# Performance work log

Hardware: AMD Instinct MI355X
Metric: run time of the kernel (lower is better)

## Reference

```python
import jax, jax.numpy as jnp
import numpy as np


def _gcn_conv(x, edge_index, W, b):
    # PyG GCNConv: linear transform, add self-loops, symmetric deg^{-1/2} norm,
    # scatter-add aggregation from source (row) into target (col), then bias.
    N = x.shape[0]
    h = x @ W  # [N, out]
    loops = jnp.arange(N, dtype=edge_index.dtype)
    row = jnp.concatenate([edge_index[0], loops])  # sources j
    col = jnp.concatenate([edge_index[1], loops])  # targets i
    deg = jax.ops.segment_sum(jnp.ones_like(col, dtype=h.dtype), col, num_segments=N)
    dinv = jnp.where(deg > 0, jax.lax.rsqrt(deg), 0.0)
    norm = dinv[row] * dinv[col]  # [E+N]
    msgs = norm[:, None] * h[row]  # gather + scale
    out = jax.ops.segment_sum(msgs, col, num_segments=N)  # scatter-add
    return out + b


def setup_inputs() -> dict:
    key = jax.random.key(0)
    k1, k2, k3, k4 = jax.random.split(key, 4)
    N, E, F, H = 100000, 3200000, 128, 64
    x = jax.random.normal(k1, (N, F), dtype=jnp.float32)
    edge_index = jax.random.randint(k2, (2, E), 0, N, dtype=jnp.int64)
    W1 = jax.random.normal(k3, (F, H), dtype=jnp.float32) * (1.0 / np.sqrt(F))
    b1 = jnp.zeros((H,), dtype=jnp.float32)
    W2 = jax.random.normal(k4, (H, 1), dtype=jnp.float32) * (1.0 / np.sqrt(H))
    b2 = jnp.zeros((1,), dtype=jnp.float32)
    return {"x": x, "edge_index": edge_index, "W1": W1, "b1": b1, "W2": W2, "b2": b2}


def reference(x, edge_index, W1, b1, W2, b2):
    # eval mode: dropout is identity
    h = _gcn_conv(x, edge_index, W1, b1)
    h = jax.nn.relu(h)
    h = _gcn_conv(h, edge_index, W2, b2)  # [N, 1]
    return jnp.mean(h, axis=0)  # [1]
```

## Files before the change

kernel.cpp:

```cpp
#include <hip/hip_runtime.h>
#include <hip/hip_bf16.h>
#include <stdint.h>


#define F_IN 128
#define H_DIM 64
#define BKT_SH 7
#define BKT_SZ 128
#define MAXBKT 1024
#define PWG 256
#define PTHR 256
#define FINBLK 2048

typedef int   i4 __attribute__((ext_vector_type(4)));
typedef float f4 __attribute__((ext_vector_type(4)));

__device__ __forceinline__ float2 bfp(unsigned int u) {
    return make_float2(__uint_as_float(u << 16), __uint_as_float(u & 0xffff0000u));
}

__global__ __launch_bounds__(PTHR) void k_hist1(const int* __restrict__ col,
                                                int* __restrict__ histG,
                                                int E, int nbkt, int chunk) {
    __shared__ int h[MAXBKT];
    for (int i = threadIdx.x; i < nbkt; i += PTHR) h[i] = 0;
    __syncthreads();
    int s = blockIdx.x * chunk, e = min(E, s + chunk);
    if (s < e) {
        int s4 = s >> 2, e4 = e >> 2;
        const i4* c4 = (const i4*)col;
        int t = s4 + threadIdx.x;
        for (; t + 3 * PTHR < e4; t += 4 * PTHR) {
            i4 a = __builtin_nontemporal_load(c4 + t);
            i4 b = __builtin_nontemporal_load(c4 + t + PTHR);
            i4 c = __builtin_nontemporal_load(c4 + t + 2 * PTHR);
            i4 d = __builtin_nontemporal_load(c4 + t + 3 * PTHR);
            atomicAdd(&h[a.x >> BKT_SH], 1); atomicAdd(&h[a.y >> BKT_SH], 1);
            atomicAdd(&h[a.z >> BKT_SH], 1); atomicAdd(&h[a.w >> BKT_SH], 1);
            atomicAdd(&h[b.x >> BKT_SH], 1); atomicAdd(&h[b.y >> BKT_SH], 1);
            atomicAdd(&h[b.z >> BKT_SH], 1); atomicAdd(&h[b.w >> BKT_SH], 1);
            atomicAdd(&h[c.x >> BKT_SH], 1); atomicAdd(&h[c.y >> BKT_SH], 1);
            atomicAdd(&h[c.z >> BKT_SH], 1); atomicAdd(&h[c.w >> BKT_SH], 1);
            atomicAdd(&h[d.x >> BKT_SH], 1); atomicAdd(&h[d.y >> BKT_SH], 1);
            atomicAdd(&h[d.z >> BKT_SH], 1); atomicAdd(&h[d.w >> BKT_SH], 1);
        }
        for (; t < e4; t += PTHR) {
            i4 a = __builtin_nontemporal_load(c4 + t);
            atomicAdd(&h[a.x >> BKT_SH], 1); atomicAdd(&h[a.y >> BKT_SH], 1);
            atomicAdd(&h[a.z >> BKT_SH], 1); atomicAdd(&h[a.w >> BKT_SH], 1);
        }
        for (int i = (e4 << 2) + threadIdx.x; i < e; i += PTHR)
            atomicAdd(&h[col[i] >> BKT_SH], 1);
    }
    __syncthreads();
    for (int i = threadIdx.x; i < nbkt; i += PTHR)
        histG[(size_t)i * PWG + blockIdx.x] = h[i];
}

__global__ __launch_bounds__(PWG) void k_hscan_a(int* __restrict__ histG,
                                                 int* __restrict__ total, int nbkt) {
    __shared__ int s[PWG];
    int b = blockIdx.x, t = threadIdx.x;
    int v = histG[(size_t)b * PWG + t];
    s[t] = v;
    __syncthreads();
    for (int d = 1; d < PWG; d <<= 1) {
        int a = (t >= d) ? s[t - d] : 0;
        __syncthreads();
        s[t] += a;
        __syncthreads();
    }
    histG[(size_t)b * PWG + t] = s[t] - v;
    if (t == PWG - 1) total[b] = s[t];
}

__global__ __launch_bounds__(1024) void k_hscan_b(const int* __restrict__ total,
                                                  int* __restrict__ bstart, int nbkt) {
    __shared__ int s[1024];
    int t = threadIdx.x;
    int v = (t < nbkt) ? total[t] : 0;
    s[t] = v;
    __syncthreads();
    for (int d = 1; d < 1024; d <<= 1) {
        int a = (t >= d) ? s[t - d] : 0;
        __syncthreads();
        s[t] += a;
        __syncthreads();
    }
    if (t < nbkt) bstart[t] = s[t] - v;
    if (t == nbkt - 1) bstart[nbkt] = s[t];
}

__global__ __launch_bounds__(PTHR) void k_part(const int* __restrict__ row,
                                               const int* __restrict__ col,
                                               const int* __restrict__ histG,
                                               const int* __restrict__ bstart,
                                               unsigned int* __restrict__ part,
                                               int E, int nbkt, int chunk) {
    __shared__ int cur[MAXBKT];
    for (int i = threadIdx.x; i < nbkt; i += PTHR)
        cur[i] = bstart[i] + histG[(size_t)i * PWG + blockIdx.x];
    __syncthreads();
    int s = blockIdx.x * chunk, e = min(E, s + chunk);
    if (s >= e) return;
    int s4 = s >> 2, e4 = e >> 2;
    const i4* c4 = (const i4*)col;
    const i4* r4 = (const i4*)row;
    int t = s4 + threadIdx.x;
    for (; t + PTHR < e4; t += 2 * PTHR) {
        i4 ca = __builtin_nontemporal_load(c4 + t);
        i4 ra = __builtin_nontemporal_load(r4 + t);
        i4 cb = __builtin_nontemporal_load(c4 + t + PTHR);
        i4 rb = __builtin_nontemporal_load(r4 + t + PTHR);
        int p;
        p = atomicAdd(&cur[ca.x >> BKT_SH], 1);
        part[p] = ((unsigned int)ra.x << BKT_SH) | (unsigned int)(ca.x & (BKT_SZ - 1));
        p = atomicAdd(&cur[ca.y >> BKT_SH], 1);
        part[p] = ((unsigned int)ra.y << BKT_SH) | (unsigned int)(ca.y & (BKT_SZ - 1));
        p = atomicAdd(&cur[ca.z >> BKT_SH], 1);
        part[p] = ((unsigned int)ra.z << BKT_SH) | (unsigned int)(ca.z & (BKT_SZ - 1));
        p = atomicAdd(&cur[ca.w >> BKT_SH], 1);
        part[p] = ((unsigned int)ra.w << BKT_SH) | (unsigned int)(ca.w & (BKT_SZ - 1));
        p = atomicAdd(&cur[cb.x >> BKT_SH], 1);
        part[p] = ((unsigned int)rb.x << BKT_SH) | (unsigned int)(cb.x & (BKT_SZ - 1));
        p = atomicAdd(&cur[cb.y >> BKT_SH], 1);
        part[p] = ((unsigned int)rb.y << BKT_SH) | (unsigned int)(cb.y & (BKT_SZ - 1));
        p = atomicAdd(&cur[cb.z >> BKT_SH], 1);
        part[p] = ((unsigned int)rb.z << BKT_SH) | (unsigned int)(cb.z & (BKT_SZ - 1));
        p = atomicAdd(&cur[cb.w >> BKT_SH], 1);
        part[p] = ((unsigned int)rb.w << BKT_SH) | (unsigned int)(cb.w & (BKT_SZ - 1));
    }
    for (; t < e4; t += PTHR) {
        i4 ca = __builtin_nontemporal_load(c4 + t);
        i4 ra = __builtin_nontemporal_load(r4 + t);
        int p;
        p = atomicAdd(&cur[ca.x >> BKT_SH], 1);
        part[p] = ((unsigned int)ra.x << BKT_SH) | (unsigned int)(ca.x & (BKT_SZ - 1));
        p = atomicAdd(&cur[ca.y >> BKT_SH], 1);
        part[p] = ((unsigned int)ra.y << BKT_SH) | (unsigned int)(ca.y & (BKT_SZ - 1));
        p = atomicAdd(&cur[ca.z >> BKT_SH], 1);
        part[p] = ((unsigned int)ra.z << BKT_SH) | (unsigned int)(ca.z & (BKT_SZ - 1));
        p = atomicAdd(&cur[ca.w >> BKT_SH], 1);
        part[p] = ((unsigned int)ra.w << BKT_SH) | (unsigned int)(ca.w & (BKT_SZ - 1));
    }
    for (int i = (e4 << 2) + threadIdx.x; i < e; i += PTHR) {
        int c = col[i], r = row[i];
        int p = atomicAdd(&cur[c >> BKT_SH], 1);
        part[p] = ((unsigned int)r << BKT_SH) | (unsigned int)(c & (BKT_SZ - 1));
    }
}

__global__ __launch_bounds__(PTHR) void k_csr(const unsigned int* __restrict__ part,
                                              const int* __restrict__ bstart,
                                              int* __restrict__ offs,
                                              float* __restrict__ dinv,
                                              int* __restrict__ csr,
                                              int N, int E, int nbkt) {
    __shared__ int dg[BKT_SZ];
    __shared__ int sc[BKT_SZ];
    __shared__ int cur[BKT_SZ];
    int b = blockIdx.x, tid = threadIdx.x;
    if (tid < BKT_SZ) dg[tid] = 0;
    __syncthreads();
    int s = bstart[b], e = bstart[b + 1];
    for (int i = s + tid; i < e; i += PTHR)
        atomicAdd(&dg[part[i] & (BKT_SZ - 1)], 1);
    __syncthreads();
    if (tid < BKT_SZ) sc[tid] = dg[tid];
    __syncthreads();
    for (int d = 1; d < BKT_SZ; d <<= 1) {
        int v = (tid < BKT_SZ && tid >= d) ? sc[tid - d] : 0;
        __syncthreads();
        if (tid < BKT_SZ) sc[tid] += v;
        __syncthreads();
    }
    if (tid < BKT_SZ) {
        int ex = sc[tid] - dg[tid];
        cur[tid] = ex;
        int g = b * BKT_SZ + tid;
        if (g < N) {
            offs[g] = s + ex;
            dinv[g] = rsqrtf((float)dg[tid] + 1.0f);
        }
    }
    if (b == 0 && tid == 0) offs[N] = E;
    __syncthreads();
    for (int i = s + tid; i < e; i += PTHR) {
        unsigned int u = part[i];
        int cl = u & (BKT_SZ - 1);
        int p = atomicAdd(&cur[cl], 1);
        csr[s + p] = u >> BKT_SH;
    }
}

__global__ __launch_bounds__(256) void k_gemm1(const float* __restrict__ x,
                                               const float* __restrict__ W1,
                                               const float* __restrict__ dinv,
                                               ushort* __restrict__ xwb, int N) {
    __shared__ float xs[64 * 132];
    __shared__ float ws[128 * 64];
    int tid = threadIdx.x;
    int row0 = blockIdx.x * 64;

    const float4* w4 = (const float4*)W1;
    float4* ws4 = (float4*)ws;
#pragma unroll
    for (int i = 0; i < 8; i++) ws4[tid + 256 * i] = w4[tid + 256 * i];

#pragma unroll
    for (int i = 0; i < 8; i++) {
        int idx = tid + 256 * i;
        int r = idx >> 5;
        int c = idx & 31;
        f4 v = {0.f, 0.f, 0.f, 0.f};
        int gr = row0 + r;
        if (gr < N) v = __builtin_nontemporal_load((const f4*)x + (size_t)gr * 32 + c);
        *(f4*)&xs[r * 132 + c * 4] = v;
    }
    __syncthreads();

    int tx = tid & 15, ty = tid >> 4;
    float acc[4][4] = {};
#pragma unroll 4
    for (int k = 0; k < 128; k++) {
        float4 wv = *(const float4*)&ws[k * 64 + tx * 4];
#pragma unroll
        for (int i = 0; i < 4; i++) {
            float xv = xs[(ty * 4 + i) * 132 + k];
            acc[i][0] += xv * wv.x;
            acc[i][1] += xv * wv.y;
            acc[i][2] += xv * wv.z;
            acc[i][3] += xv * wv.w;
        }
    }
#pragma unroll
    for (int i = 0; i < 4; i++) {
        int gr = row0 + ty * 4 + i;
        if (gr < N) {
            float dsc = dinv[gr];
            __hip_bfloat16 q0 = __float2bfloat16(acc[i][0] * dsc);
            __hip_bfloat16 q1 = __float2bfloat16(acc[i][1] * dsc);
            __hip_bfloat16 q2 = __float2bfloat16(acc[i][2] * dsc);
            __hip_bfloat16 q3 = __float2bfloat16(acc[i][3] * dsc);
            ushort4 o = make_ushort4(*(ushort*)&q0, *(ushort*)&q1,
                                     *(ushort*)&q2, *(ushort*)&q3);
            *(ushort4*)&xwb[(size_t)gr * 64 + tx * 4] = o;
        }
    }
}

__global__ __launch_bounds__(256) void k_agg(const ushort* __restrict__ xws,
                                             const int* __restrict__ csr,
                                             const int* __restrict__ offs,
                                             const float* __restrict__ dinv,
                                             const float* __restrict__ b1,
                                             const float* __restrict__ W2,
                                             float* __restrict__ yp, int N) {
    int wid = (blockIdx.x * blockDim.x + threadIdx.x) >> 6;
    int lane = threadIdx.x & 63;
    if (wid >= N) return;
    int m = lane & 15, g = lane >> 4;
    const uint2* xw4 = (const uint2*)xws;

    float di = dinv[wid];
    float a0 = 0.f, a1 = 0.f, a2 = 0.f, a3 = 0.f;
    if (g == 0) {
        uint2 u = xw4[(size_t)wid * 16 + m];
        float2 w0 = bfp(u.x), w1 = bfp(u.y);
        a0 += w0.x; a1 += w0.y; a2 += w1.x; a3 += w1.y;
    }
    int p = offs[wid], pe = offs[wid + 1];
    for (; p + 32 <= pe; p += 32) {
        int j[8]; uint2 u[8];
#pragma unroll
        for (int q = 0; q < 8; q++) j[q] = csr[p + 4 * q + g];
#pragma unroll
        for (int q = 0; q < 8; q++) u[q] = xw4[(size_t)j[q] * 16 + m];
#pragma unroll
        for (int q = 0; q < 8; q++) {
            float2 w0 = bfp(u[q].x), w1 = bfp(u[q].y);
            a0 += w0.x; a1 += w0.y; a2 += w1.x; a3 += w1.y;
        }
    }
    for (; p + 8 <= pe; p += 8) {
        int ja = csr[p + g], jb = csr[p + 4 + g];
        uint2 ua = xw4[(size_t)ja * 16 + m];
        uint2 ub = xw4[(size_t)jb * 16 + m];
        float2 w0 = bfp(ua.x), w1 = bfp(ua.y);
        float2 w2 = bfp(ub.x), w3 = bfp(ub.y);
        a0 += w0.x + w2.x; a1 += w0.y + w2.y;
        a2 += w1.x + w3.x; a3 += w1.y + w3.y;
    }
    for (; p + 4 <= pe; p += 4) {
        int j = csr[p + g];
        uint2 u = xw4[(size_t)j * 16 + m];
        float2 w0 = bfp(u.x), w1 = bfp(u.y);
        a0 += w0.x; a1 += w0.y; a2 += w1.x; a3 += w1.y;
    }
    int rem = pe - p;
    if (g < rem) {
        int j = csr[p + g];
        uint2 u = xw4[(size_t)j * 16 + m];
        float2 w0 = bfp(u.x), w1 = bfp(u.y);
        a0 += w0.x; a1 += w0.y; a2 += w1.x; a3 += w1.y;
    }
    a0 += __shfl_xor(a0, 16, 64); a0 += __shfl_xor(a0, 32, 64);
    a1 += __shfl_xor(a1, 16, 64); a1 += __shfl_xor(a1, 32, 64);
    a2 += __shfl_xor(a2, 16, 64); a2 += __shfl_xor(a2, 32, 64);
    a3 += __shfl_xor(a3, 16, 64); a3 += __shfl_xor(a3, 32, 64);
    float4 bv = ((const float4*)b1)[m];
    float4 wv = ((const float4*)W2)[m];
    float h0 = fmaxf(bv.x + di * a0, 0.f);
    float h1 = fmaxf(bv.y + di * a1, 0.f);
    float h2 = fmaxf(bv.z + di * a2, 0.f);
    float h3 = fmaxf(bv.w + di * a3, 0.f);
    float v = h0 * wv.x + h1 * wv.y + h2 * wv.z + h3 * wv.w;
    v += __shfl_xor(v, 1, 64);
    v += __shfl_xor(v, 2, 64);
    v += __shfl_xor(v, 4, 64);
    v += __shfl_xor(v, 8, 64);
    if (lane == 0) yp[wid] = di * v;
}

__global__ __launch_bounds__(256) void k_final2(const int* __restrict__ csr,
                                                const int* __restrict__ offs,
                                                const float* __restrict__ dinv,
                                                const float* __restrict__ yp,
                                                float* __restrict__ partial, int N) {
    int lane = threadIdx.x & 63, w = threadIdx.x >> 6;
    int nwave_tot = gridDim.x * 4;
    int wid0 = blockIdx.x * 4 + w;
    float wpart = 0.f;
    for (int i = wid0; i < N; i += nwave_tot) {
        int p0 = offs[i], p1 = offs[i + 1];
        float s = (lane == 0) ? yp[i] : 0.f;
        for (int p = p0 + lane; p < p1; p += 64)
            s += yp[csr[p]];
#pragma unroll
        for (int d = 32; d > 0; d >>= 1) s += __shfl_xor(s, d, 64);
        if (lane == 0) wpart += dinv[i] * s;
    }
    __shared__ float wsum[4];
    if (lane == 0) wsum[w] = wpart;
    __syncthreads();
    if (threadIdx.x == 0)
        partial[blockIdx.x] = (wsum[0] + wsum[1]) + (wsum[2] + wsum[3]);
}

__global__ __launch_bounds__(256) void k_write(const float* __restrict__ partial,
                                               const float* __restrict__ b2,
                                               float* __restrict__ out, int nb, int N) {
    float s = 0.f;
    for (int i = threadIdx.x; i < nb; i += 256) s += partial[i];
#pragma unroll
    for (int d = 32; d > 0; d >>= 1) s += __shfl_xor(s, d, 64);
    __shared__ float wsum[4];
    int lane = threadIdx.x & 63, w = threadIdx.x >> 6;
    if (lane == 0) wsum[w] = s;
    __syncthreads();
    if (threadIdx.x == 0)
        out[0] = b2[0] + ((wsum[0] + wsum[1]) + (wsum[2] + wsum[3])) / (float)N;
}

extern "C" void kernel_launch(void* const* d_in, const int* in_sizes, int n_in,
                              void* d_out, int out_size, void* d_ws, size_t ws_size,
                              hipStream_t stream) {
    const float* x  = (const float*)d_in[0];
    const int*   ei = (const int*)d_in[1];
    const float* W1 = (const float*)d_in[2];
    const float* b1 = (const float*)d_in[3];
    const float* W2 = (const float*)d_in[4];
    const float* b2 = (const float*)d_in[5];

    int N = in_sizes[0] / F_IN;
    int E = in_sizes[1] / 2;
    const int* erow = ei;
    const int* ecol = ei + E;

    int NBKT = (N + BKT_SZ - 1) >> BKT_SH;
    int chunk = (((E + PWG - 1) / PWG) + 3) & ~3;

    char* w = (char*)d_ws;
    auto take = [&](size_t bytes) {
        char* p = w;
        w += (bytes + 255) & ~(size_t)255;
        return p;
    };
    int*          histG   = (int*)take((size_t)NBKT * PWG * 4);
    int*          total   = (int*)take((size_t)NBKT * 4);
    int*          bstart  = (int*)take((size_t)(NBKT + 1) * 4);
    unsigned int* part    = (unsigned int*)take((size_t)E * 4);
    int*          csr     = (int*)take((size_t)E * 4);
    int*          offs    = (int*)take((size_t)(N + 1) * 4);
    float*        dinv    = (float*)take((size_t)N * 4);
    float*        yp      = (float*)take((size_t)N * 4);
    float*        partial = (float*)take((size_t)FINBLK * 4);
    ushort*       xwb     = (ushort*)take((size_t)N * H_DIM * 2);
    (void)ws_size;

    float* out = (float*)d_out;

    k_hist1<<<PWG, PTHR, 0, stream>>>(ecol, histG, E, NBKT, chunk);
    k_hscan_a<<<NBKT, PWG, 0, stream>>>(histG, total, NBKT);
    k_hscan_b<<<1, 1024, 0, stream>>>(total, bstart, NBKT);
    k_part<<<PWG, PTHR, 0, stream>>>(erow, ecol, histG, bstart, part, E, NBKT, chunk);
    k_csr<<<NBKT, PTHR, 0, stream>>>(part, bstart, offs, dinv, csr, N, E, NBKT);
    k_gemm1<<<(N + 63) / 64, 256, 0, stream>>>(x, W1, dinv, xwb, N);
    k_agg<<<((size_t)N * 64 + 255) / 256, 256, 0, stream>>>(xwb, csr, offs, dinv, b1, W2, yp, N);
    k_final2<<<FINBLK, 256, 0, stream>>>(csr, offs, dinv, yp, partial, N);
    k_write<<<1, 256, 0, stream>>>(partial, b2, out, FINBLK, N);
}
```

Baseline: 217.2 us.

## Split hidden features into two halves and aggregate each in a separate pass

The GEMM writes the bf16 hidden features as two separate 32-wide column arrays, and the aggregation kernel runs twice, once per half, so each pass gathers from a 6.4 MB table instead of 12.8 MB. The intent is to raise cache hit rates for the random neighbour gathers. In exchange the CSR index array and offsets are read twice, an extra kernel launch and temporary buffer are added, and each lane now handles 8 neighbours per step with 64-byte row segments.

```diff
diff --git a/kernel.cpp b/kernel.cpp
--- a/kernel.cpp
+++ b/kernel.cpp
@@ -196,7 +196,8 @@
 __global__ __launch_bounds__(256) void k_gemm1(const float* __restrict__ x,
                                                const float* __restrict__ W1,
                                                const float* __restrict__ dinv,
-                                               ushort* __restrict__ xwb, int N) {
+                                               ushort* __restrict__ xwb0,
+                                               ushort* __restrict__ xwb1, int N) {
     __shared__ float xs[64 * 132];
     __shared__ float ws[128 * 64];
     int tid = threadIdx.x;
@@ -233,6 +234,8 @@
             acc[i][3] += xv * wv.w;
         }
     }
+    ushort* dst = (tx < 8) ? xwb0 : xwb1;
+    int txl = tx & 7;
 #pragma unroll
     for (int i = 0; i < 4; i++) {
         int gr = row0 + ty * 4 + i;
@@ -244,72 +247,65 @@
             __hip_bfloat16 q3 = __float2bfloat16(acc[i][3] * dsc);
             ushort4 o = make_ushort4(*(ushort*)&q0, *(ushort*)&q1,
                                      *(ushort*)&q2, *(ushort*)&q3);
-            *(ushort4*)&xwb[(size_t)gr * 64 + tx * 4] = o;
-        }
-    }
-}
-
-__global__ __launch_bounds__(256) void k_agg(const ushort* __restrict__ xws,
+            *(ushort4*)&dst[(size_t)gr * 32 + txl * 4] = o;
+        }
+    }
+}
+
+template<int P>
+__global__ __launch_bounds__(256) void k_agg(const ushort* __restrict__ xwp,
                                              const int* __restrict__ csr,
                                              const int* __restrict__ offs,
                                              const float* __restrict__ dinv,
                                              const float* __restrict__ b1,
                                              const float* __restrict__ W2,
+                                             float* __restrict__ tmpv,
                                              float* __restrict__ yp, int N) {
     int wid = (blockIdx.x * blockDim.x + threadIdx.x) >> 6;
     int lane = threadIdx.x & 63;
     if (wid >= N) return;
-    int m = lane & 15, g = lane >> 4;
-    const uint2* xw4 = (const uint2*)xws;
+    int m = lane & 7, g = lane >> 3;
+    const uint2* xw = (const uint2*)xwp;
 
     float di = dinv[wid];
     float a0 = 0.f, a1 = 0.f, a2 = 0.f, a3 = 0.f;
     if (g == 0) {
-        uint2 u = xw4[(size_t)wid * 16 + m];
+        uint2 u = xw[(size_t)wid * 8 + m];
         float2 w0 = bfp(u.x), w1 = bfp(u.y);
         a0 += w0.x; a1 += w0.y; a2 += w1.x; a3 += w1.y;
     }
     int p = offs[wid], pe = offs[wid + 1];
     for (; p + 32 <= pe; p += 32) {
-        int j[8]; uint2 u[8];
-#pragma unroll
-        for (int q = 0; q < 8; q++) j[q] = csr[p + 4 * q + g];
-#pragma unroll
-        for (int q = 0; q < 8; q++) u[q] = xw4[(size_t)j[q] * 16 + m];
-#pragma unroll
-        for (int q = 0; q < 8; q++) {
+        int j[4]; uint2 u[4];
+#pragma unroll
+        for (int q = 0; q < 4; q++) j[q] = csr[p + 8 * q + g];
+#pragma unroll
+        for (int q = 0; q < 4; q++) u[q] = xw[(size_t)j[q] * 8 + m];
+#pragma unroll
+        for (int q = 0; q < 4; q++) {
             float2 w0 = bfp(u[q].x), w1 = bfp(u[q].y);
             a0 += w0.x; a1 += w0.y; a2 += w1.x; a3 += w1.y;
         }
     }
     for (; p + 8 <= pe; p += 8) {
-        int ja = csr[p + g], jb = csr[p + 4 + g];
-        uint2 ua = xw4[(size_t)ja * 16 + m];
-        uint2 ub = xw4[(size_t)jb * 16 + m];
-        float2 w0 = bfp(ua.x), w1 = bfp(ua.y);
-        float2 w2 = bfp(ub.x), w3 = bfp(ub.y);
-        a0 += w0.x + w2.x; a1 += w0.y + w2.y;
-        a2 += w1.x + w3.x; a3 += w1.y + w3.y;
-    }
-    for (; p + 4 <= pe; p += 4) {
         int j = csr[p + g];
-        uint2 u = xw4[(size_t)j * 16 + m];
+        uint2 u = xw[(size_t)j * 8 + m];
         float2 w0 = bfp(u.x), w1 = bfp(u.y);
         a0 += w0.x; a1 += w0.y; a2 += w1.x; a3 += w1.y;
     }
     int rem = pe - p;
     if (g < rem) {
         int j = csr[p + g];
-        uint2 u = xw4[(size_t)j * 16 + m];
+        uint2 u = xw[(size_t)j * 8 + m];
         float2 w0 = bfp(u.x), w1 = bfp(u.y);
         a0 += w0.x; a1 += w0.y; a2 += w1.x; a3 += w1.y;
     }
-    a0 += __shfl_xor(a0, 16, 64); a0 += __shfl_xor(a0, 32, 64);
-    a1 += __shfl_xor(a1, 16, 64); a1 += __shfl_xor(a1, 32, 64);
-    a2 += __shfl_xor(a2, 16, 64); a2 += __shfl_xor(a2, 32, 64);
-    a3 += __shfl_xor(a3, 16, 64); a3 += __shfl_xor(a3, 32, 64);
-    float4 bv = ((const float4*)b1)[m];
-    float4 wv = ((const float4*)W2)[m];
+    a0 += __shfl_xor(a0, 8, 64); a0 += __shfl_xor(a0, 16, 64); a0 += __shfl_xor(a0, 32, 64);
+    a1 += __shfl_xor(a1, 8, 64); a1 += __shfl_xor(a1, 16, 64); a1 += __shfl_xor(a1, 32, 64);
+    a2 += __shfl_xor(a2, 8, 64); a2 += __shfl_xor(a2, 16, 64); a2 += __shfl_xor(a2, 32, 64);
+    a3 += __shfl_xor(a3, 8, 64); a3 += __shfl_xor(a3, 16, 64); a3 += __shfl_xor(a3, 32, 64);
+    float4 bv = ((const float4*)b1)[P * 8 + m];
+    float4 wv = ((const float4*)W2)[P * 8 + m];
     float h0 = fmaxf(bv.x + di * a0, 0.f);
     float h1 = fmaxf(bv.y + di * a1, 0.f);
     float h2 = fmaxf(bv.z + di * a2, 0.f);
@@ -318,8 +314,10 @@
     v += __shfl_xor(v, 1, 64);
     v += __shfl_xor(v, 2, 64);
     v += __shfl_xor(v, 4, 64);
-    v += __shfl_xor(v, 8, 64);
-    if (lane == 0) yp[wid] = di * v;
+    if (lane == 0) {
+        if (P == 0) tmpv[wid] = v;
+        else        yp[wid] = di * (tmpv[wid] + v);
+    }
 }
 
 __global__ __launch_bounds__(256) void k_final2(const int* __restrict__ csr,
@@ -394,8 +392,10 @@
     int*          offs    = (int*)take((size_t)(N + 1) * 4);
     float*        dinv    = (float*)take((size_t)N * 4);
     float*        yp      = (float*)take((size_t)N * 4);
+    float*        tmpv    = (float*)take((size_t)N * 4);
     float*        partial = (float*)take((size_t)FINBLK * 4);
-    ushort*       xwb     = (ushort*)take((size_t)N * H_DIM * 2);
+    ushort*       xwb0    = (ushort*)take((size_t)N * 32 * 2);
+    ushort*       xwb1    = (ushort*)take((size_t)N * 32 * 2);
     (void)ws_size;
 
     float* out = (float*)d_out;
@@ -405,8 +405,10 @@
     k_hscan_b<<<1, 1024, 0, stream>>>(total, bstart, NBKT);
     k_part<<<PWG, PTHR, 0, stream>>>(erow, ecol, histG, bstart, part, E, NBKT, chunk);
     k_csr<<<NBKT, PTHR, 0, stream>>>(part, bstart, offs, dinv, csr, N, E, NBKT);
-    k_gemm1<<<(N + 63) / 64, 256, 0, stream>>>(x, W1, dinv, xwb, N);
-    k_agg<<<((size_t)N * 64 + 255) / 256, 256, 0, stream>>>(xwb, csr, offs, dinv, b1, W2, yp, N);
+    k_gemm1<<<(N + 63) / 64, 256, 0, stream>>>(x, W1, dinv, xwb0, xwb1, N);
+    int aggGrid = ((size_t)N * 64 + 255) / 256;
+    k_agg<0><<<aggGrid, 256, 0, stream>>>(xwb0, csr, offs, dinv, b1, W2, tmpv, yp, N);
+    k_agg<1><<<aggGrid, 256, 0, stream>>>(xwb1, csr, offs, dinv, b1, W2, tmpv, yp, N);
     k_final2<<<FINBLK, 256, 0, stream>>>(csr, offs, dinv, yp, partial, N);
     k_write<<<1, 256, 0, stream>>>(partial, b2, out, FINBLK, N);
 }
```

After: 254.3 us. 1.17x slower.
